# Kernel tuning notes

Measured on AMD Instinct MI355X. Metric: run time of the kernel, lower is better.

The kernel has to match this reference:

```python
import jax, jax.numpy as jnp
import numpy as np


def _chamfer_sum_mean(x, y):
    # x: [B, N, 3], y: [B, M, 3]
    # squared pairwise distances [B, N, M]
    d2 = (
        jnp.sum(x * x, axis=-1)[:, :, None]
        + jnp.sum(y * y, axis=-1)[:, None, :]
        - 2.0 * jnp.einsum('bnd,bmd->bnm', x, y)
    )
    cham_x = jnp.sum(jnp.min(d2, axis=2), axis=1)  # sum over N of NN dist in y
    cham_y = jnp.sum(jnp.min(d2, axis=1), axis=1)  # sum over M of NN dist in x
    # point_reduction='sum', batch_reduction='mean'
    return jnp.mean(cham_x) + jnp.mean(cham_y)


def setup_inputs() -> dict:
    key = jax.random.key(0)
    k1, k2 = jax.random.split(key)
    B, V, N, D = 8, 4, 2048, 3
    X_v = jax.random.normal(k1, (B, V, N, D), dtype=jnp.float32)
    target_X_v = jax.random.normal(k2, (B, V, N, D), dtype=jnp.float32)
    return {"X_v": X_v, "target_X_v": target_X_v}


def reference(X_v, target_X_v):
    # per-view chamfer losses, vectorized over the view axis (dim 1)
    per_view = jax.vmap(_chamfer_sum_mean, in_axes=(1, 1))(X_v, target_X_v)  # [V]
    # original code: loss = cd(view 0); then loop adds cd(view idx) for all idx
    # => view 0 is counted twice (faithful to source).
    return per_view[0] + jnp.sum(per_view)
```

## Files before the change

### kernel.cpp

```cpp
#include <hip/hip_runtime.h>


#define B_ 8
#define V_ 4
#define N_ 2048
#define JOBS 64
#define RPB 256
#define GRID_ (JOBS * (N_ / RPB))
#define CHUNK 512
#define NCHUNK (N_ / CHUNK)
#define CPITCH 24

typedef short bf16x8 __attribute__((ext_vector_type(8)));
typedef float f32x16 __attribute__((ext_vector_type(16)));

__device__ __forceinline__ unsigned short f2bf(float f) {
  union { float f; unsigned u; } v; v.f = f;
  const unsigned r = v.u + 0x7fffu + ((v.u >> 16) & 1u);
  return (unsigned short)(r >> 16);
}
__device__ __forceinline__ float bf2f(unsigned short h) {
  union { unsigned u; float f; } v; v.u = ((unsigned)h) << 16;
  return v.f;
}

__device__ __forceinline__ void pack_col(float y0, float y1, float y2,
                                         unsigned short* dst) {
  const unsigned short h0 = f2bf(y0), h1 = f2bf(y1), h2 = f2bf(y2);
  const unsigned short l0 = f2bf(y0 - bf2f(h0));
  const unsigned short l1 = f2bf(y1 - bf2f(h1));
  const unsigned short l2 = f2bf(y2 - bf2f(h2));
  const float w = -0.5f * fmaf(y0, y0, fmaf(y1, y1, y2 * y2));
  const unsigned short wh = f2bf(w);
  const unsigned short wl = f2bf(w - bf2f(wh));
  bf16x8 b0, b1;
  b0[0] = (short)h0; b0[1] = (short)h1; b0[2] = (short)h2;
  b0[3] = (short)l0; b0[4] = (short)l1; b0[5] = (short)l2;
  b0[6] = (short)h0; b0[7] = (short)h1;
  b1[0] = (short)h2;
  b1[1] = (short)wh; b1[2] = (short)wl;
  b1[3] = (short)l0; b1[4] = (short)l1; b1[5] = (short)l2;
  b1[6] = 0; b1[7] = 0;
  *(bf16x8*)(dst) = b0;
  *(bf16x8*)(dst + 8) = b1;
}

__device__ __forceinline__ void stage_chunk(const float* __restrict__ yb,
                                            unsigned short* __restrict__ dstbuf,
                                            int ch, int t) {
  const int c0 = ch * CHUNK + t * 2;
  const float2* yp2 = (const float2*)(yb + (size_t)c0 * 3);
  const float2 u0 = yp2[0], u1 = yp2[1], u2 = yp2[2];
  unsigned short* dst = dstbuf + (size_t)(t * 2) * CPITCH;
  pack_col(u0.x, u0.y, u1.x, dst);
  pack_col(u1.y, u2.x, u2.y, dst + CPITCH);
}

__global__ __launch_bounds__(256, 2) void chamfer_main(
    const float* __restrict__ X, const float* __restrict__ T,
    float* __restrict__ bsum) {
  __shared__ unsigned short yf[2][CHUNK * CPITCH];
  __shared__ float red4[4];

  const int p = blockIdx.x;
  const int bid = (p & 7) * (GRID_ / 8) + (p >> 3);
  const int job = bid >> 3;
  const int rc  = bid & 7;
  const int pair = job >> 1;
  const int dir  = job & 1;
  const float* xb = (dir ? T : X) + (size_t)pair * N_ * 3;
  const float* yb = (dir ? X : T) + (size_t)pair * N_ * 3;
  const int t = threadIdx.x;
  const int lane = t & 63;
  const int wv = t >> 6;
  const int lr = lane & 31;
  const int g  = lane >> 5;

  bf16x8 afrag[2];
  float xn2[2];
  const int rbase = rc * RPB + wv * 64;
#pragma unroll
  for (int rt = 0; rt < 2; ++rt) {
    const int r = rbase + rt * 32 + lr;
    const float x0 = xb[r * 3 + 0], x1 = xb[r * 3 + 1], x2 = xb[r * 3 + 2];
    xn2[rt] = fmaf(x0, x0, fmaf(x1, x1, x2 * x2));
    const unsigned short h0 = f2bf(x0), h1 = f2bf(x1), h2 = f2bf(x2);
    const unsigned short l0 = f2bf(x0 - bf2f(h0));
    const unsigned short l1 = f2bf(x1 - bf2f(h1));
    const unsigned short l2 = f2bf(x2 - bf2f(h2));
    const unsigned short ONE = 0x3F80;
    bf16x8 a;
    if (g == 0) {
      a[0] = (short)h0; a[1] = (short)h1; a[2] = (short)h2;
      a[3] = (short)h0; a[4] = (short)h1; a[5] = (short)h2;
      a[6] = (short)l0; a[7] = (short)l1;
    } else {
      a[0] = (short)l2; a[1] = (short)ONE; a[2] = (short)ONE;
      a[3] = (short)l0; a[4] = (short)l1; a[5] = (short)l2;
      a[6] = 0; a[7] = 0;
    }
    afrag[rt] = a;
  }

  f32x16 r0, r1;
#pragma unroll
  for (int j = 0; j < 16; ++j) { r0[j] = -1e30f; r1[j] = -1e30f; }

  stage_chunk(yb, yf[0], 0, t);
  __syncthreads();

  for (int ch = 0; ch < NCHUNK; ++ch) {
    if (ch + 1 < NCHUNK)
      stage_chunk(yb, yf[(ch + 1) & 1], ch + 1, t);
    const unsigned short* yfb = yf[ch & 1];
#pragma unroll
    for (int pr = 0; pr < CHUNK / 64; ++pr) {
      const unsigned short* pa = yfb + (size_t)(pr * 64 + lr) * CPITCH + g * 8;
      const bf16x8 bA = *(const bf16x8*)pa;
      const bf16x8 bB = *(const bf16x8*)(pa + 32 * CPITCH);
      const f32x16 d00 =
          __builtin_amdgcn_mfma_f32_32x32x16_bf16(afrag[0], bA, (f32x16){}, 0, 0, 0);
      const f32x16 d10 =
          __builtin_amdgcn_mfma_f32_32x32x16_bf16(afrag[1], bA, (f32x16){}, 0, 0, 0);
      const f32x16 d01 =
          __builtin_amdgcn_mfma_f32_32x32x16_bf16(afrag[0], bB, (f32x16){}, 0, 0, 0);
      const f32x16 d11 =
          __builtin_amdgcn_mfma_f32_32x32x16_bf16(afrag[1], bB, (f32x16){}, 0, 0, 0);
#pragma unroll
      for (int j = 0; j < 16; ++j) {
        r0[j] = fmaxf(fmaxf(r0[j], d00[j]), d01[j]);
        r1[j] = fmaxf(fmaxf(r1[j], d10[j]), d11[j]);
      }
    }
    __syncthreads();
  }

  float acc = 0.0f;
#pragma unroll
  for (int rt = 0; rt < 2; ++rt) {
#pragma unroll
    for (int j = 0; j < 16; ++j) {
      float m = rt ? r1[j] : r0[j];
      m = fmaxf(m, __shfl_xor(m, 1, 64));
      m = fmaxf(m, __shfl_xor(m, 2, 64));
      m = fmaxf(m, __shfl_xor(m, 4, 64));
      m = fmaxf(m, __shfl_xor(m, 8, 64));
      m = fmaxf(m, __shfl_xor(m, 16, 64));
      const int rl = (j & 3) + 8 * (j >> 2) + 4 * g;
      if (lr == rl) acc += fmaf(-2.0f, m, xn2[rt]);
    }
  }
  const int v_ = pair & (V_ - 1);
  acc *= ((v_ == 0) ? 2.0f : 1.0f) * (1.0f / (float)B_);
#pragma unroll
  for (int o = 32; o > 0; o >>= 1) acc += __shfl_down(acc, o, 64);
  if (lane == 0) red4[wv] = acc;
  __syncthreads();
  if (t == 0) bsum[bid] = (red4[0] + red4[1]) + (red4[2] + red4[3]);
}

__global__ __launch_bounds__(256) void chamfer_final(
    const float* __restrict__ bsum, float* __restrict__ out) {
  __shared__ float red4[4];
  const int t = threadIdx.x;
  float v = bsum[t] + bsum[t + 256];
#pragma unroll
  for (int o = 32; o > 0; o >>= 1) v += __shfl_down(v, o, 64);
  const int lane = t & 63, wid = t >> 6;
  if (lane == 0) red4[wid] = v;
  __syncthreads();
  if (t == 0) out[0] = (red4[0] + red4[1]) + (red4[2] + red4[3]);
}

extern "C" void kernel_launch(void* const* d_in, const int* in_sizes, int n_in,
                              void* d_out, int out_size, void* d_ws, size_t ws_size,
                              hipStream_t stream) {
  const float* X = (const float*)d_in[0];
  const float* T = (const float*)d_in[1];
  float* out = (float*)d_out;
  float* bsum = (float*)d_ws;

  chamfer_main<<<GRID_, 256, 0, stream>>>(X, T, bsum);
  chamfer_final<<<1, 256, 0, stream>>>(bsum, out);
}
```

Baseline: 20.35 us.

## Pre-pack target points in separate kernel and bulk-load full panel into LDS

Adds a pack_y kernel that converts every target point cloud once into the split-bf16 MFMA column format in workspace, so the main kernel no longer repacks the y points in each block. The main kernel now uses 512-thread blocks, each covering 512 rows, and loads the whole 2048-column packed panel into LDS (96 KB) with global_load_lds before one barrier. This removes the chunked double-buffer loop and its per-chunk barriers. In exchange it adds a kernel launch, a workspace round trip, larger LDS use that limits occupancy, and half as many blocks.

Measured after the change: 26.67 us. 1.31x slower.

```diff
diff --git a/kernel.cpp b/kernel.cpp
--- a/kernel.cpp
+++ b/kernel.cpp
@@ -5,11 +5,10 @@
 #define V_ 4
 #define N_ 2048
 #define JOBS 64
-#define RPB 256
+#define RPB 512
 #define GRID_ (JOBS * (N_ / RPB))
-#define CHUNK 512
-#define NCHUNK (N_ / CHUNK)
 #define CPITCH 24
+#define PANEL_BYTES (N_ * CPITCH * 2)
 
 typedef short bf16x8 __attribute__((ext_vector_type(8)));
 typedef float f32x16 __attribute__((ext_vector_type(16)));
@@ -45,36 +44,49 @@
   *(bf16x8*)(dst + 8) = b1;
 }
 
-__device__ __forceinline__ void stage_chunk(const float* __restrict__ yb,
-                                            unsigned short* __restrict__ dstbuf,
-                                            int ch, int t) {
-  const int c0 = ch * CHUNK + t * 2;
-  const float2* yp2 = (const float2*)(yb + (size_t)c0 * 3);
-  const float2 u0 = yp2[0], u1 = yp2[1], u2 = yp2[2];
-  unsigned short* dst = dstbuf + (size_t)(t * 2) * CPITCH;
-  pack_col(u0.x, u0.y, u1.x, dst);
-  pack_col(u1.y, u2.x, u2.y, dst + CPITCH);
+__global__ __launch_bounds__(256) void pack_y(
+    const float* __restrict__ X, const float* __restrict__ T,
+    unsigned short* __restrict__ P) {
+  const int tid = blockIdx.x * 256 + threadIdx.x;
+  const int panel = tid >> 11;
+  const int col = tid & (N_ - 1);
+  const int pair = panel >> 1;
+  const float* src = ((panel & 1) ? T : X) + (size_t)pair * N_ * 3 + col * 3;
+  pack_col(src[0], src[1], src[2], P + (size_t)tid * CPITCH);
 }
 
-__global__ __launch_bounds__(256, 2) void chamfer_main(
+__global__ __launch_bounds__(512, 2) void chamfer_main(
     const float* __restrict__ X, const float* __restrict__ T,
-    float* __restrict__ bsum) {
-  __shared__ unsigned short yf[2][CHUNK * CPITCH];
-  __shared__ float red4[4];
+    const unsigned short* __restrict__ P, float* __restrict__ bsum) {
+  __shared__ unsigned short yl[N_ * CPITCH];
+  __shared__ float red8[8];
 
   const int p = blockIdx.x;
   const int bid = (p & 7) * (GRID_ / 8) + (p >> 3);
-  const int job = bid >> 3;
-  const int rc  = bid & 7;
+  const int job = bid >> 2;
+  const int rc  = bid & 3;
   const int pair = job >> 1;
   const int dir  = job & 1;
   const float* xb = (dir ? T : X) + (size_t)pair * N_ * 3;
-  const float* yb = (dir ? X : T) + (size_t)pair * N_ * 3;
+  const unsigned short* Pb =
+      P + ((size_t)((pair << 1) | (dir ^ 1))) * N_ * CPITCH;
   const int t = threadIdx.x;
   const int lane = t & 63;
   const int wv = t >> 6;
   const int lr = lane & 31;
   const int g  = lane >> 5;
+
+  {
+    const char* gsrc = (const char*)Pb + wv * 12288 + lane * 16;
+    char* ldst = (char*)yl + wv * 12288;
+#pragma unroll
+    for (int i = 0; i < 12; ++i) {
+      __builtin_amdgcn_global_load_lds(
+          (const __attribute__((address_space(1))) unsigned int*)(gsrc + i * 1024),
+          (__attribute__((address_space(3))) unsigned int*)(ldst + i * 1024),
+          16, 0, 0);
+    }
+  }
 
   bf16x8 afrag[2];
   float xn2[2];
@@ -106,33 +118,26 @@
 #pragma unroll
   for (int j = 0; j < 16; ++j) { r0[j] = -1e30f; r1[j] = -1e30f; }
 
-  stage_chunk(yb, yf[0], 0, t);
   __syncthreads();
 
-  for (int ch = 0; ch < NCHUNK; ++ch) {
-    if (ch + 1 < NCHUNK)
-      stage_chunk(yb, yf[(ch + 1) & 1], ch + 1, t);
-    const unsigned short* yfb = yf[ch & 1];
+#pragma unroll 4
+  for (int ct = 0; ct < 32; ++ct) {
+    const unsigned short* pa = yl + (size_t)(ct * 64 + lr) * CPITCH + g * 8;
+    const bf16x8 bA = *(const bf16x8*)pa;
+    const bf16x8 bB = *(const bf16x8*)(pa + 32 * CPITCH);
+    const f32x16 d00 =
+        __builtin_amdgcn_mfma_f32_32x32x16_bf16(afrag[0], bA, (f32x16){}, 0, 0, 0);
+    const f32x16 d01 =
+        __builtin_amdgcn_mfma_f32_32x32x16_bf16(afrag[0], bB, (f32x16){}, 0, 0, 0);
+    const f32x16 d10 =
+        __builtin_amdgcn_mfma_f32_32x32x16_bf16(afrag[1], bA, (f32x16){}, 0, 0, 0);
+    const f32x16 d11 =
+        __builtin_amdgcn_mfma_f32_32x32x16_bf16(afrag[1], bB, (f32x16){}, 0, 0, 0);
 #pragma unroll
-    for (int pr = 0; pr < CHUNK / 64; ++pr) {
-      const unsigned short* pa = yfb + (size_t)(pr * 64 + lr) * CPITCH + g * 8;
-      const bf16x8 bA = *(const bf16x8*)pa;
-      const bf16x8 bB = *(const bf16x8*)(pa + 32 * CPITCH);
-      const f32x16 d00 =
-          __builtin_amdgcn_mfma_f32_32x32x16_bf16(afrag[0], bA, (f32x16){}, 0, 0, 0);
-      const f32x16 d10 =
-          __builtin_amdgcn_mfma_f32_32x32x16_bf16(afrag[1], bA, (f32x16){}, 0, 0, 0);
-      const f32x16 d01 =
-          __builtin_amdgcn_mfma_f32_32x32x16_bf16(afrag[0], bB, (f32x16){}, 0, 0, 0);
-      const f32x16 d11 =
-          __builtin_amdgcn_mfma_f32_32x32x16_bf16(afrag[1], bB, (f32x16){}, 0, 0, 0);
-#pragma unroll
-      for (int j = 0; j < 16; ++j) {
-        r0[j] = fmaxf(fmaxf(r0[j], d00[j]), d01[j]);
-        r1[j] = fmaxf(fmaxf(r1[j], d10[j]), d11[j]);
-      }
+    for (int j = 0; j < 16; ++j) {
+      r0[j] = fmaxf(fmaxf(r0[j], d00[j]), d01[j]);
+      r1[j] = fmaxf(fmaxf(r1[j], d10[j]), d11[j]);
     }
-    __syncthreads();
   }
 
   float acc = 0.0f;
@@ -154,16 +159,21 @@
   acc *= ((v_ == 0) ? 2.0f : 1.0f) * (1.0f / (float)B_);
 #pragma unroll
   for (int o = 32; o > 0; o >>= 1) acc += __shfl_down(acc, o, 64);
-  if (lane == 0) red4[wv] = acc;
+  if (lane == 0) red8[wv] = acc;
   __syncthreads();
-  if (t == 0) bsum[bid] = (red4[0] + red4[1]) + (red4[2] + red4[3]);
+  if (t == 0) {
+    float s = 0.0f;
+#pragma unroll
+    for (int i = 0; i < 8; ++i) s += red8[i];
+    bsum[bid] = s;
+  }
 }
 
 __global__ __launch_bounds__(256) void chamfer_final(
     const float* __restrict__ bsum, float* __restrict__ out) {
   __shared__ float red4[4];
   const int t = threadIdx.x;
-  float v = bsum[t] + bsum[t + 256];
+  float v = bsum[t];
 #pragma unroll
   for (int o = 32; o > 0; o >>= 1) v += __shfl_down(v, o, 64);
   const int lane = t & 63, wid = t >> 6;
@@ -178,8 +188,10 @@
   const float* X = (const float*)d_in[0];
   const float* T = (const float*)d_in[1];
   float* out = (float*)d_out;
-  float* bsum = (float*)d_ws;
+  unsigned short* P = (unsigned short*)d_ws;
+  float* bsum = (float*)((char*)d_ws + (size_t)JOBS * PANEL_BYTES);
 
-  chamfer_main<<<GRID_, 256, 0, stream>>>(X, T, bsum);
+  pack_y<<<(JOBS * N_) / 256, 256, 0, stream>>>(X, T, P);
+  chamfer_main<<<GRID_, 512, 0, stream>>>(X, T, P, bsum);
   chamfer_final<<<1, 256, 0, stream>>>(bsum, out);
 }
```
